# Optimization experiments

Measured on AMD Instinct MI355X. Metric: run time of the kernel, lower is better.

Reference implementation:

```python
import jax, jax.numpy as jnp
import numpy as np

N = 262144
DIM = 256
NUM_HEADS = 4
HEAD_DIM = DIM // NUM_HEADS
B = 4096
SCALE = HEAD_DIM ** (-0.5)
EPS = 1e-8


def setup_inputs() -> dict:
    key = jax.random.key(0)
    ks = jax.random.split(key, 7)
    x = jax.random.normal(ks[0], (N, DIM), dtype=jnp.float32)
    batch = jnp.sort(jax.random.randint(ks[1], (N,), 0, B)).astype(jnp.int64)
    query = jax.random.normal(ks[2], (NUM_HEADS, HEAD_DIM), dtype=jnp.float32)
    # nn.Linear default init scale ~ 1/sqrt(dim); keep exp() well-behaved
    key_w = jax.random.normal(ks[3], (DIM, DIM), dtype=jnp.float32) / np.sqrt(DIM)
    key_b = jax.random.normal(ks[4], (DIM,), dtype=jnp.float32) * 0.01
    value_w = jax.random.normal(ks[5], (DIM, DIM), dtype=jnp.float32) / np.sqrt(DIM)
    value_b = jax.random.normal(ks[6], (DIM,), dtype=jnp.float32) * 0.01
    return {"x": x, "batch": batch, "query": query, "key_w": key_w,
            "key_b": key_b, "value_w": value_w, "value_b": value_b}


def reference(x, batch, query, key_w, key_b, value_w, value_b):
    # k, v: [N, H, Hd]  (torch Linear: x @ W.T + b)
    k = (x @ key_w.T + key_b).reshape(N, NUM_HEADS, HEAD_DIM)
    v = (x @ value_w.T + value_b).reshape(N, NUM_HEADS, HEAD_DIM)
    # attn: [N, H] -- dot of learned per-head query with each node's key
    attn = jnp.einsum('hd,nhd->nh', query, k) * SCALE
    attn_exp = jnp.exp(attn)  # faithful: no max-subtraction in original
    # segment softmax denominator gathered back to nodes: [N, H]
    attn_sum = jax.ops.segment_sum(attn_exp, batch, num_segments=B)[batch]
    attn_norm = attn_exp / (attn_sum + EPS)
    # weighted values scatter-added per segment: [B, H, Hd]
    weighted = attn_norm[:, :, None] * v
    pooled = jax.ops.segment_sum(weighted, batch, num_segments=B)
    return pooled.reshape(B, DIM)
```

## Files before the change

kernel.cpp:

```cpp
#include <hip/hip_runtime.h>
#include <hip/hip_bf16.h>


constexpr int DIM = 256;
constexpr int NH  = 4;
constexpr int HD  = 64;
constexpr float SCL  = 0.125f;
constexpr float EPSV = 1e-8f;

__global__ void prep_qw(const float* __restrict__ query,
                        const float* __restrict__ key_w,
                        const float* __restrict__ key_b,
                        float* __restrict__ ws){
  int t = blockIdx.x * 256 + threadIdx.x;
  int h = t >> 8, j = t & 255;
  float acc = 0.f;
  for (int d = 0; d < HD; ++d)
    acc += query[h*HD+d] * key_w[(size_t)(h*HD+d)*DIM + j];
  ws[t] = acc;
  if (j == 0){
    float bb = 0.f;
    for (int d = 0; d < HD; ++d)
      bb += query[h*HD+d] * key_b[h*HD+d];
    ws[1024 + h] = bb;
  }
}

__global__ void seg_offsets(const int* __restrict__ batch32,
                            int* __restrict__ offs, int N, int B){
  int i = blockIdx.x * 256 + threadIdx.x;
  if (i >= N) return;
  const bool is64 = (batch32[N-1] == 0);
  int v  = is64 ? batch32[2*i] : batch32[i];
  int vp = (i == 0) ? -1 : (is64 ? batch32[2*(i-1)] : batch32[i-1]);
  for (int b = vp + 1; b <= v; ++b) offs[b] = i;
  if (i == N-1)
    for (int b = v + 1; b <= B; ++b) offs[b] = N;
}

__global__ __launch_bounds__(256, 4)
void attn_pool(const float* __restrict__ x,
               const int* __restrict__ offs,
               const float* __restrict__ value_w,
               const float* __restrict__ value_b,
               const float* __restrict__ ws,
               float* __restrict__ out){
  __shared__ __align__(16) float S_all[4][NH][DIM];
  __shared__ __align__(16) float Sfin[NH][DIM];
  __shared__ float sums_all[4][NH];
  __shared__ float invs[NH], wsums[NH];

  const int b   = blockIdx.x;
  const int tid = threadIdx.x;

  const int seg_start = offs[b];
  const int seg_end   = offs[b+1];

  const int wave = tid >> 6, lane = tid & 63;
  const int half = lane >> 5, sl = lane & 31;

  float qwr[NH][8];
  #pragma unroll
  for (int h = 0; h < NH; ++h){
    const float4* q4 = (const float4*)(ws + h*DIM + sl*8);
    float4 a = q4[0], c = q4[1];
    qwr[h][0]=a.x; qwr[h][1]=a.y; qwr[h][2]=a.z; qwr[h][3]=a.w;
    qwr[h][4]=c.x; qwr[h][5]=c.y; qwr[h][6]=c.z; qwr[h][7]=c.w;
  }
  float qb[NH];
  #pragma unroll
  for (int h = 0; h < NH; ++h) qb[h] = ws[1024 + h];

  float Sacc[NH][8];
  #pragma unroll
  for (int h = 0; h < NH; ++h)
    #pragma unroll
    for (int c = 0; c < 8; ++c) Sacc[h][c] = 0.f;
  float se[NH] = {0.f, 0.f, 0.f, 0.f};

  const float4* xr4 = (const float4*)x;

  for (int n = seg_start + wave*2 + half; n < seg_end; n += 8){
    float4 ra = xr4[(size_t)n * 64 + sl*2];
    float4 rb = xr4[(size_t)n * 64 + sl*2 + 1];
    float xv[8];
    xv[0]=ra.x; xv[1]=ra.y; xv[2]=ra.z; xv[3]=ra.w;
    xv[4]=rb.x; xv[5]=rb.y; xv[6]=rb.z; xv[7]=rb.w;

    float p[NH];
    #pragma unroll
    for (int h = 0; h < NH; ++h){
      float a = 0.f;
      #pragma unroll
      for (int c = 0; c < 8; ++c) a += qwr[h][c] * xv[c];
      p[h] = a;
    }
    #pragma unroll
    for (int m = 1; m < 32; m <<= 1){
      #pragma unroll
      for (int h = 0; h < NH; ++h) p[h] += __shfl_xor(p[h], m, 64);
    }
    float e[NH];
    #pragma unroll
    for (int h = 0; h < NH; ++h){
      e[h] = __expf((p[h] + qb[h]) * SCL);
      se[h] += e[h];
    }
    #pragma unroll
    for (int h = 0; h < NH; ++h)
      #pragma unroll
      for (int c = 0; c < 8; ++c) Sacc[h][c] += e[h] * xv[c];
  }

  #pragma unroll
  for (int h = 0; h < NH; ++h){
    se[h] += __shfl_xor(se[h], 32, 64);
    #pragma unroll
    for (int c = 0; c < 8; ++c) Sacc[h][c] += __shfl_xor(Sacc[h][c], 32, 64);
  }
  if (half == 0){
    #pragma unroll
    for (int h = 0; h < NH; ++h){
      float4 lo = make_float4(Sacc[h][0], Sacc[h][1], Sacc[h][2], Sacc[h][3]);
      float4 hi = make_float4(Sacc[h][4], Sacc[h][5], Sacc[h][6], Sacc[h][7]);
      float4* dst = (float4*)&S_all[wave][h][sl*8];
      dst[0] = lo; dst[1] = hi;
    }
    if (sl == 0){
      #pragma unroll
      for (int h = 0; h < NH; ++h) sums_all[wave][h] = se[h];
    }
  }
  __syncthreads();

  #pragma unroll
  for (int h = 0; h < NH; ++h)
    Sfin[h][tid] = S_all[0][h][tid] + S_all[1][h][tid] + S_all[2][h][tid] + S_all[3][h][tid];
  if (tid < NH){
    float tot = sums_all[0][tid] + sums_all[1][tid] + sums_all[2][tid] + sums_all[3][tid];
    float inv = 1.f / (tot + EPSV);
    invs[tid]  = inv;
    wsums[tid] = tot * inv;
  }
  __syncthreads();

  const int h = tid >> 6;
  const float inv = invs[h], wsm = wsums[h];
  const float4* vrow = (const float4*)(value_w + (size_t)tid * DIM);
  const float4* sp   = (const float4*)&Sfin[h][0];
  float acc = 0.f;
  #pragma unroll
  for (int q = 0; q < 64; ++q){
    float4 r = vrow[q];
    float4 s = sp[q];
    acc += r.x*s.x + r.y*s.y + r.z*s.z + r.w*s.w;
  }
  out[(size_t)b * DIM + tid] = acc * inv + wsm * value_b[tid];
}

extern "C" void kernel_launch(void* const* d_in, const int* in_sizes, int n_in,
                              void* d_out, int out_size, void* d_ws, size_t ws_size,
                              hipStream_t stream){
  const float* x       = (const float*)d_in[0];
  const int*   batch   = (const int*)d_in[1];
  const float* query   = (const float*)d_in[2];
  const float* key_w   = (const float*)d_in[3];
  const float* key_b   = (const float*)d_in[4];
  const float* value_w = (const float*)d_in[5];
  const float* value_b = (const float*)d_in[6];
  float* ws  = (float*)d_ws;
  int*   offs = (int*)(ws + 1088);
  float* out = (float*)d_out;

  const int N = in_sizes[1];
  const int B = out_size / DIM;

  prep_qw<<<4, 256, 0, stream>>>(query, key_w, key_b, ws);
  seg_offsets<<<(N + 255) / 256, 256, 0, stream>>>(batch, offs, N, B);
  attn_pool<<<B, 256, 0, stream>>>(x, offs, value_w, value_b, ws, out);
}
```

Before: 472.0 us.

## Double block size to 512 threads, process two rows per half-wave, split epilogue

Each segment block now uses 512 threads (8 waves). Each half-wave handles two rows per iteration with interleaved loads and reductions, which gives more independent memory requests and better latency hiding. The final value_w projection is split across two thread halves and combined through shared memory. In exchange the kernel carries more registers per thread (two x rows live), uses more shared memory for the 8-wave partial sums, and adds an extra reduction and barrier.

```diff
diff --git a/kernel.cpp b/kernel.cpp
--- a/kernel.cpp
+++ b/kernel.cpp
@@ -38,26 +38,27 @@
     for (int b = v + 1; b <= B; ++b) offs[b] = N;
 }
 
-__global__ __launch_bounds__(256, 4)
+__global__ __launch_bounds__(512, 4)
 void attn_pool(const float* __restrict__ x,
                const int* __restrict__ offs,
                const float* __restrict__ value_w,
                const float* __restrict__ value_b,
                const float* __restrict__ ws,
                float* __restrict__ out){
-  __shared__ __align__(16) float S_all[4][NH][DIM];
+  __shared__ __align__(16) float S_all[8][NH][DIM];
   __shared__ __align__(16) float Sfin[NH][DIM];
-  __shared__ float sums_all[4][NH];
+  __shared__ __align__(16) float ep[2][DIM];
+  __shared__ float sums_all[8][NH];
   __shared__ float invs[NH], wsums[NH];
 
   const int b   = blockIdx.x;
   const int tid = threadIdx.x;
-
   const int seg_start = offs[b];
   const int seg_end   = offs[b+1];
 
   const int wave = tid >> 6, lane = tid & 63;
   const int half = lane >> 5, sl = lane & 31;
+  const int sigma = wave * 2 + half;
 
   float qwr[NH][8];
   #pragma unroll
@@ -80,36 +81,43 @@
 
   const float4* xr4 = (const float4*)x;
 
-  for (int n = seg_start + wave*2 + half; n < seg_end; n += 8){
-    float4 ra = xr4[(size_t)n * 64 + sl*2];
-    float4 rb = xr4[(size_t)n * 64 + sl*2 + 1];
-    float xv[8];
-    xv[0]=ra.x; xv[1]=ra.y; xv[2]=ra.z; xv[3]=ra.w;
-    xv[4]=rb.x; xv[5]=rb.y; xv[6]=rb.z; xv[7]=rb.w;
+  for (int n0 = seg_start + sigma*2; n0 < seg_end; n0 += 32){
+    const int n1 = n0 + 1;
+    const bool has1 = (n1 < seg_end);
+    float4 a0 = xr4[(size_t)n0 * 64 + sl*2];
+    float4 b0 = xr4[(size_t)n0 * 64 + sl*2 + 1];
+    float4 a1 = make_float4(0.f,0.f,0.f,0.f), b1 = a1;
+    if (has1){ a1 = xr4[(size_t)n1 * 64 + sl*2]; b1 = xr4[(size_t)n1 * 64 + sl*2 + 1]; }
 
-    float p[NH];
+    float xv0[8] = {a0.x,a0.y,a0.z,a0.w,b0.x,b0.y,b0.z,b0.w};
+    float xv1[8] = {a1.x,a1.y,a1.z,a1.w,b1.x,b1.y,b1.z,b1.w};
+
+    float p0[NH], p1[NH];
     #pragma unroll
     for (int h = 0; h < NH; ++h){
-      float a = 0.f;
+      float s0 = 0.f, s1 = 0.f;
       #pragma unroll
-      for (int c = 0; c < 8; ++c) a += qwr[h][c] * xv[c];
-      p[h] = a;
+      for (int c = 0; c < 8; ++c){ s0 += qwr[h][c]*xv0[c]; s1 += qwr[h][c]*xv1[c]; }
+      p0[h] = s0; p1[h] = s1;
     }
     #pragma unroll
     for (int m = 1; m < 32; m <<= 1){
       #pragma unroll
-      for (int h = 0; h < NH; ++h) p[h] += __shfl_xor(p[h], m, 64);
+      for (int h = 0; h < NH; ++h){
+        p0[h] += __shfl_xor(p0[h], m, 64);
+        p1[h] += __shfl_xor(p1[h], m, 64);
+      }
     }
-    float e[NH];
+    const float g1 = has1 ? 1.f : 0.f;
     #pragma unroll
     for (int h = 0; h < NH; ++h){
-      e[h] = __expf((p[h] + qb[h]) * SCL);
-      se[h] += e[h];
+      float e0 = __expf((p0[h] + qb[h]) * SCL);
+      float e1 = __expf((p1[h] + qb[h]) * SCL) * g1;
+      se[h] += e0 + e1;
+      #pragma unroll
+      for (int c = 0; c < 8; ++c)
+        Sacc[h][c] += e0*xv0[c] + e1*xv1[c];
     }
-    #pragma unroll
-    for (int h = 0; h < NH; ++h)
-      #pragma unroll
-      for (int c = 0; c < 8; ++c) Sacc[h][c] += e[h] * xv[c];
   }
 
   #pragma unroll
@@ -134,28 +142,38 @@
   __syncthreads();
 
   #pragma unroll
-  for (int h = 0; h < NH; ++h)
-    Sfin[h][tid] = S_all[0][h][tid] + S_all[1][h][tid] + S_all[2][h][tid] + S_all[3][h][tid];
+  for (int idx = tid; idx < NH*DIM; idx += 512){
+    int h = idx >> 8, c = idx & 255;
+    float s = 0.f;
+    #pragma unroll
+    for (int w = 0; w < 8; ++w) s += S_all[w][h][c];
+    Sfin[h][c] = s;
+  }
   if (tid < NH){
-    float tot = sums_all[0][tid] + sums_all[1][tid] + sums_all[2][tid] + sums_all[3][tid];
+    float tot = 0.f;
+    #pragma unroll
+    for (int w = 0; w < 8; ++w) tot += sums_all[w][tid];
     float inv = 1.f / (tot + EPSV);
     invs[tid]  = inv;
     wsums[tid] = tot * inv;
   }
   __syncthreads();
 
-  const int h = tid >> 6;
-  const float inv = invs[h], wsm = wsums[h];
-  const float4* vrow = (const float4*)(value_w + (size_t)tid * DIM);
-  const float4* sp   = (const float4*)&Sfin[h][0];
+  const int t = tid & 255, part = tid >> 8;
+  const int h = t >> 6;
+  const float4* vrow = (const float4*)(value_w + (size_t)t * DIM) + part*32;
+  const float4* sp   = (const float4*)&Sfin[h][0] + part*32;
   float acc = 0.f;
   #pragma unroll
-  for (int q = 0; q < 64; ++q){
+  for (int q = 0; q < 32; ++q){
     float4 r = vrow[q];
     float4 s = sp[q];
     acc += r.x*s.x + r.y*s.y + r.z*s.z + r.w*s.w;
   }
-  out[(size_t)b * DIM + tid] = acc * inv + wsm * value_b[tid];
+  ep[part][t] = acc;
+  __syncthreads();
+  if (part == 0)
+    out[(size_t)b * DIM + t] = (ep[0][t] + ep[1][t]) * invs[h] + wsums[h] * value_b[t];
 }
 
 extern "C" void kernel_launch(void* const* d_in, const int* in_sizes, int n_in,
@@ -177,5 +195,5 @@
 
   prep_qw<<<4, 256, 0, stream>>>(query, key_w, key_b, ws);
   seg_offsets<<<(N + 255) / 256, 256, 0, stream>>>(batch, offs, N, B);
-  attn_pool<<<B, 256, 0, stream>>>(x, offs, value_w, value_b, ws, out);
+  attn_pool<<<B, 512, 0, stream>>>(x, offs, value_w, value_b, ws, out);
 }
```

Measured after the change: 466.6 us. Within noise of the previous version (-1.1%).
